# Kernel tuning notes

Measured on AMD Instinct MI355X. Metric: run time of the kernel, lower is better.

The kernel has to match this reference:

```python
import jax, jax.numpy as jnp
import numpy as np

N_ENT = 50000
N_REL = 500
DIM = 256
BATCH = 512
EPS = 1e-5


def setup_inputs() -> dict:
    key = jax.random.key(0)
    ks = jax.random.split(key, 5)
    E_emb = jax.random.normal(ks[0], (4, N_ENT, DIM), jnp.float32)   # (a_re, a_im, b_re, b_im)
    R_emb = jax.random.normal(ks[1], (4, N_REL, DIM), jnp.float32)
    psi_emb = jax.random.normal(ks[2], (N_REL, DIM), jnp.float32)
    bn_gamma = jnp.ones((4, DIM), jnp.float32)
    bn_beta = jnp.zeros((4, DIM), jnp.float32)
    biases = jnp.zeros((4, N_ENT), jnp.float32)                      # b_a, b_x, b_y, b_z
    h_idx = jax.random.randint(ks[3], (BATCH,), 0, N_ENT)
    r_idx = jax.random.randint(ks[4], (BATCH,), 0, N_REL)
    return dict(E_emb=E_emb, R_emb=R_emb, psi_emb=psi_emb, bn_gamma=bn_gamma,
                bn_beta=bn_beta, biases=biases, h_idx=h_idx, r_idx=r_idx)


def _qnorm(q):
    # QubitNorm: normalize so |a|^2 + |b|^2 = 1 per embedding coordinate.
    # q: [4, ..., d] stacked real parts.
    length = jnp.sqrt(jnp.sum(q * q, axis=0, keepdims=True))
    return q / length


def _bn(q, gamma, beta):
    # QubitBatchNorm1d (training-mode batch stats), per component and per feature.
    # q: [4, B, d]
    mean = q.mean(axis=1, keepdims=True)
    var = q.var(axis=1, keepdims=True)
    return (q - mean) / jnp.sqrt(var + EPS) * gamma[:, None, :] + beta[:, None, :]


def _cmul(a, b):
    return (a[0] * b[0] - a[1] * b[1], a[0] * b[1] + a[1] * b[0])


def reference(E_emb, R_emb, psi_emb, bn_gamma, bn_beta, biases, h_idx, r_idx):
    # h = E_bn(norm(E(h_idx)))
    h = _bn(_qnorm(E_emb[:, h_idx]), bn_gamma, bn_beta)   # [4, B, d]
    # r = norm(R(r_idx))
    r = _qnorm(R_emb[:, r_idx])                           # [4, B, d]
    psi = psi_emb[r_idx]                                  # [B, d]
    z = (jnp.cos(psi), jnp.sin(psi))
    h_a, h_b = (h[0], h[1]), (h[2], h[3])
    r_a, r_b = (r[0], r[1]), (r[2], r[3])
    ra_conj = (r[0], -r[1])
    rb_conj = (r[2], -r[3])
    # QubitMult: a = h_a*r_a - z*(h_b*conj(r_b)); b = h_a*r_b + z*(h_b*conj(r_a))
    m1 = _cmul(h_a, r_a)
    m2 = _cmul(z, _cmul(h_b, rb_conj))
    m3 = _cmul(h_a, r_b)
    m4 = _cmul(z, _cmul(h_b, ra_conj))
    t = jnp.stack([m1[0] - m2[0], m1[1] - m2[1], m3[0] + m4[0], m3[1] + m4[1]])  # [4, B, d]
    # All-entity table: E_bn(norm(E))
    E = _bn(_qnorm(E_emb), bn_gamma, bn_beta)             # [4, N, d]
    # QubitScoringAll: per-component dot product against all entities (dropout = eval identity)
    scores = jnp.einsum('cbd,cnd->cbn', t, E)             # [4, B, N]
    y = jax.nn.sigmoid(scores + biases[:, None, :])       # (y_a, y_ai, y_b, y_bi) stacked
    return y
```

## Files before the change

### kernel.cpp

```cpp
#include <hip/hip_runtime.h>
#include <math.h>

#define NENT 50000
#define NREL 500
#define DIM 256
#define BATCH 512
#define EPSV 1e-5f

#define WS_ACC    0
#define WS_STATS  4096
#define WS_KC     8192
#define WS_F16    10240

typedef _Float16 f16x8 __attribute__((ext_vector_type(8)));
typedef _Float16 f16x4 __attribute__((ext_vector_type(4)));
typedef float f32x4 __attribute__((ext_vector_type(4)));
typedef float f32x16 __attribute__((ext_vector_type(16)));

__device__ inline f32x16 zero16() {
    f32x16 v;
#pragma unroll
    for (int i = 0; i < 16; ++i) v[i] = 0.f;
    return v;
}

__global__ void convert_stats_kernel(const float* __restrict__ E, _Float16* __restrict__ Eh,
                                     float* __restrict__ acc) {
    __shared__ float red[3][64][33];
    int tid = threadIdx.x;
    int dq = tid & 63, j = tid >> 6;
    int d0 = dq * 4;
    int per = (NENT + gridDim.x - 1) / gridDim.x;
    int n0 = blockIdx.x * per;
    int n1 = n0 + per; if (n1 > NENT) n1 = NENT;

    float sm[4][4]; float sq[4][4];
#pragma unroll
    for (int c = 0; c < 4; ++c)
#pragma unroll
        for (int dd = 0; dd < 4; ++dd) { sm[c][dd] = 0.f; sq[c][dd] = 0.f; }

    for (int n = n0 + j; n < n1; n += 4) {
        size_t ga = (size_t)n * DIM + d0;
        f32x4 e[4];
        e[0] = *(const f32x4*)(E + ga);
        e[1] = *(const f32x4*)(E + (size_t)NENT * DIM + ga);
        e[2] = *(const f32x4*)(E + (size_t)2 * NENT * DIM + ga);
        e[3] = *(const f32x4*)(E + (size_t)3 * NENT * DIM + ga);
        float inv[4];
#pragma unroll
        for (int dd = 0; dd < 4; ++dd)
            inv[dd] = rsqrtf(e[0][dd]*e[0][dd] + e[1][dd]*e[1][dd] +
                             e[2][dd]*e[2][dd] + e[3][dd]*e[3][dd]);
#pragma unroll
        for (int c = 0; c < 4; ++c) {
            f16x4 hv;
#pragma unroll
            for (int dd = 0; dd < 4; ++dd) {
                float v = e[c][dd] * inv[dd];
                hv[dd] = (_Float16)v;
                sm[c][dd] += v; sq[c][dd] += v * v;
            }
            *(f16x4*)(Eh + (size_t)c * NENT * DIM + ga) = hv;
        }
    }

    if (j > 0) {
        float* p = &red[j-1][dq][0];
#pragma unroll
        for (int c = 0; c < 4; ++c)
#pragma unroll
            for (int dd = 0; dd < 4; ++dd) {
                p[c*4 + dd]      = sm[c][dd];
                p[16 + c*4 + dd] = sq[c][dd];
            }
    }
    __syncthreads();
    if (j == 0) {
#pragma unroll
        for (int c = 0; c < 4; ++c)
#pragma unroll
            for (int dd = 0; dd < 4; ++dd) {
                float s = sm[c][dd] + red[0][dq][c*4+dd] + red[1][dq][c*4+dd] + red[2][dq][c*4+dd];
                float q = sq[c][dd] + red[0][dq][16+c*4+dd] + red[1][dq][16+c*4+dd] + red[2][dq][16+c*4+dd];
                atomicAdd(&acc[c*DIM + d0 + dd], s);
                atomicAdd(&acc[1024 + c*DIM + d0 + dd], q);
            }
    }
}

__global__ void stats_batch_kernel(const float* __restrict__ E, const int* __restrict__ h_idx,
                                   float* __restrict__ accH) {
    int d = threadIdx.x;
    int b0 = blockIdx.x * 32;
    float sm0=0,sm1=0,sm2=0,sm3=0, sq0=0,sq1=0,sq2=0,sq3=0;
    for (int j = 0; j < 32; ++j) {
        int n = h_idx[b0 + j];
        int ga = n*DIM + d;
        float e0 = E[ga];
        float e1 = E[1*NENT*DIM + ga];
        float e2 = E[2*NENT*DIM + ga];
        float e3 = E[3*NENT*DIM + ga];
        float inv = rsqrtf(e0*e0+e1*e1+e2*e2+e3*e3);
        e0*=inv; e1*=inv; e2*=inv; e3*=inv;
        sm0+=e0; sq0+=e0*e0;
        sm1+=e1; sq1+=e1*e1;
        sm2+=e2; sq2+=e2*e2;
        sm3+=e3; sq3+=e3*e3;
    }
    atomicAdd(&accH[0*DIM+d], sm0); atomicAdd(&accH[1024 + 0*DIM+d], sq0);
    atomicAdd(&accH[1*DIM+d], sm1); atomicAdd(&accH[1024 + 1*DIM+d], sq1);
    atomicAdd(&accH[2*DIM+d], sm2); atomicAdd(&accH[1024 + 2*DIM+d], sq2);
    atomicAdd(&accH[3*DIM+d], sm3); atomicAdd(&accH[1024 + 3*DIM+d], sq3);
}

__global__ void finalize_stats_kernel(const float* __restrict__ acc, float* __restrict__ stats) {
    int i = blockIdx.x * blockDim.x + threadIdx.x;
    float mE = acc[i] * (1.0f / NENT);
    float vE = acc[1024 + i] * (1.0f / NENT) - mE * mE;
    float mH = acc[2048 + i] * (1.0f / BATCH);
    float vH = acc[3072 + i] * (1.0f / BATCH) - mH * mH;
    stats[i]        = mE;
    stats[1024 + i] = rsqrtf(vE + EPSV);
    stats[2048 + i] = mH;
    stats[3072 + i] = rsqrtf(vH + EPSV);
}

__global__ void build_t_kernel(const float* __restrict__ E, const float* __restrict__ R,
                               const float* __restrict__ psi_emb,
                               const float* __restrict__ gamma, const float* __restrict__ beta,
                               const int* __restrict__ h_idx, const int* __restrict__ r_idx,
                               const float* __restrict__ stats,
                               _Float16* __restrict__ th, float* __restrict__ Kc) {
    __shared__ float red[4];
    int b = blockIdx.x, d = threadIdx.x;
    int wave = d >> 6, lane = d & 63;
    int hn = h_idx[b], rn = r_idx[b];

    float hv[4];
    hv[0] = E[hn*DIM + d];
    hv[1] = E[1*NENT*DIM + hn*DIM + d];
    hv[2] = E[2*NENT*DIM + hn*DIM + d];
    hv[3] = E[3*NENT*DIM + hn*DIM + d];
    float invh = rsqrtf(hv[0]*hv[0]+hv[1]*hv[1]+hv[2]*hv[2]+hv[3]*hv[3]);
    float hq[4];
#pragma unroll
    for (int c = 0; c < 4; ++c) {
        float v = hv[c] * invh;
        float mH = stats[2048 + c*DIM + d], isH = stats[3072 + c*DIM + d];
        hq[c] = (v - mH) * isH * gamma[c*DIM + d] + beta[c*DIM + d];
    }

    float r0 = R[rn*DIM + d];
    float r1 = R[1*NREL*DIM + rn*DIM + d];
    float r2 = R[2*NREL*DIM + rn*DIM + d];
    float r3 = R[3*NREL*DIM + rn*DIM + d];
    float invr = rsqrtf(r0*r0+r1*r1+r2*r2+r3*r3);
    r0*=invr; r1*=invr; r2*=invr; r3*=invr;

    float p = psi_emb[rn*DIM + d];
    float cz = cosf(p), sz = sinf(p);

    float m1r = hq[0]*r0 - hq[1]*r1;
    float m1i = hq[0]*r1 + hq[1]*r0;
    float X   = hq[2]*r2 + hq[3]*r3;
    float Y   = hq[3]*r2 - hq[2]*r3;
    float m2r = cz*X - sz*Y;
    float m2i = cz*Y + sz*X;
    float m3r = hq[0]*r2 - hq[1]*r3;
    float m3i = hq[0]*r3 + hq[1]*r2;
    float U   = hq[2]*r0 + hq[3]*r1;
    float V   = hq[3]*r0 - hq[2]*r1;
    float m4r = cz*U - sz*V;
    float m4i = cz*V + sz*U;

    float t[4] = { m1r - m2r, m1i - m2i, m3r + m4r, m3i + m4i };

#pragma unroll
    for (int c = 0; c < 4; ++c) {
        float g   = gamma[c*DIM + d];
        float mE  = stats[c*DIM + d];
        float isE = stats[1024 + c*DIM + d];
        th[((size_t)c*BATCH + b)*DIM + d] = (_Float16)(t[c] * g * isE);
        float kp = t[c] * (beta[c*DIM + d] - g * mE * isE);
#pragma unroll
        for (int off = 32; off > 0; off >>= 1) kp += __shfl_down(kp, off, 64);
        if (lane == 0) red[wave] = kp;
        __syncthreads();
        if (d == 0) Kc[c*BATCH + b] = red[0] + red[1] + red[2] + red[3];
        __syncthreads();
    }
}

__launch_bounds__(256)
__global__ void score_gemm_kernel(const _Float16* __restrict__ th,
                                  const _Float16* __restrict__ Eh,
                                  const float* __restrict__ Kc,
                                  const float* __restrict__ biases,
                                  float* __restrict__ out) {
    __shared__ __align__(1024) char smem[32768];
    int tid = threadIdx.x;
    int w = tid >> 6, l = tid & 63;
    int lr = l & 31, lh = l >> 5;
    int wm = w & 1, wn = w >> 1;

    int lin = blockIdx.x + (int)gridDim.x * (blockIdx.y + (int)gridDim.y * blockIdx.z);
    int wg  = (lin & 7) * 782 + (lin >> 3);
    int bt  = wg & 3;
    int nt  = (wg >> 2) % 391;
    int c   = wg / 1564;
    int b0  = bt * 128;
    int n0  = nt * 128;

    const _Float16* Ah = th + (size_t)c * BATCH * DIM;
    const _Float16* Bh = Eh + (size_t)c * NENT * DIM;

    f32x16 acc00 = zero16(), acc01 = zero16(), acc10 = zero16(), acc11 = zero16();

    auto stage = [&](int kc, int slot) {
        int kbase = kc * 32;
#pragma unroll
        for (int i = 0; i < 4; ++i) {
            int f = w * 4 + i;
            const _Float16* gp;
            if (f < 8) {
                int mf = f >> 1, ks = f & 1;
                gp = Ah + (size_t)(b0 + mf*32 + lr) * DIM + kbase + ks*16 + lh*8;
            } else {
                int g = f - 8, nf = g >> 1, ks = g & 1;
                int n = n0 + nf*32 + lr; if (n > NENT-1) n = NENT-1;
                gp = Bh + (size_t)n * DIM + kbase + ks*16 + lh*8;
            }
            __builtin_amdgcn_global_load_lds(
                (const __attribute__((address_space(1))) void*)gp,
                (__attribute__((address_space(3))) void*)(smem + slot * 16384 + f * 1024),
                16, 0, 0);
        }
    };

    auto compute = [&](int slot) {
        const char* s = smem + slot * 16384;
#pragma unroll
        for (int ks = 0; ks < 2; ++ks) {
            f16x8 a0  = *(const f16x8*)(s + ((wm*2+0)*2 + ks)*1024 + l*16);
            f16x8 a1  = *(const f16x8*)(s + ((wm*2+1)*2 + ks)*1024 + l*16);
            f16x8 bb0 = *(const f16x8*)(s + 8192 + ((wn*2+0)*2 + ks)*1024 + l*16);
            f16x8 bb1 = *(const f16x8*)(s + 8192 + ((wn*2+1)*2 + ks)*1024 + l*16);
            acc00 = __builtin_amdgcn_mfma_f32_32x32x16_f16(a0, bb0, acc00, 0, 0, 0);
            acc01 = __builtin_amdgcn_mfma_f32_32x32x16_f16(a0, bb1, acc01, 0, 0, 0);
            acc10 = __builtin_amdgcn_mfma_f32_32x32x16_f16(a1, bb0, acc10, 0, 0, 0);
            acc11 = __builtin_amdgcn_mfma_f32_32x32x16_f16(a1, bb1, acc11, 0, 0, 0);
        }
    };

    stage(0, 0);
    for (int t = 0; t < 7; ++t) {
        stage(t + 1, (t + 1) & 1);
        asm volatile("s_waitcnt vmcnt(4)" ::: "memory");
        __builtin_amdgcn_s_barrier();
        compute(t & 1);
        __builtin_amdgcn_s_barrier();
    }
    asm volatile("s_waitcnt vmcnt(0)" ::: "memory");
    __builtin_amdgcn_s_barrier();
    compute(1);

    const float* Kcc = Kc + c * BATCH;
    const float* bc  = biases + (size_t)c * NENT;
    float* oc = out + (size_t)c * BATCH * NENT;
#pragma unroll
    for (int mi = 0; mi < 2; ++mi) {
#pragma unroll
        for (int ni = 0; ni < 2; ++ni) {
            const f32x16& a = (mi==0) ? (ni==0 ? acc00 : acc01) : (ni==0 ? acc10 : acc11);
            int n = n0 + wn*64 + ni*32 + lr;
            bool ok = (n < NENT);
            float bv = ok ? bc[n] : 0.f;
#pragma unroll
            for (int reg = 0; reg < 16; ++reg) {
                int m = b0 + wm*64 + mi*32 + (reg & 3) + 8*(reg >> 2) + 4*lh;
                float x = a[reg] + Kcc[m] + bv;
                if (ok) oc[(size_t)m * NENT + n] = 1.f / (1.f + __expf(-x));
            }
        }
    }
}

extern "C" void kernel_launch(void* const* d_in, const int* in_sizes, int n_in,
                              void* d_out, int out_size, void* d_ws, size_t ws_size,
                              hipStream_t stream) {
    const float* E      = (const float*)d_in[0];
    const float* R      = (const float*)d_in[1];
    const float* psi    = (const float*)d_in[2];
    const float* gamma  = (const float*)d_in[3];
    const float* beta   = (const float*)d_in[4];
    const float* biases = (const float*)d_in[5];
    const int* h_idx    = (const int*)d_in[6];
    const int* r_idx    = (const int*)d_in[7];
    float* out = (float*)d_out;
    float* ws  = (float*)d_ws;

    _Float16* th = (_Float16*)(ws + WS_F16);
    _Float16* Eh = th + (size_t)4 * BATCH * DIM;

    hipMemsetAsync(ws + WS_ACC, 0, 4096 * sizeof(float), stream);

    convert_stats_kernel<<<512, 256, 0, stream>>>(E, Eh, ws + WS_ACC);
    stats_batch_kernel<<<16, 256, 0, stream>>>(E, h_idx, ws + WS_ACC + 2048);
    finalize_stats_kernel<<<4, 256, 0, stream>>>(ws + WS_ACC, ws + WS_STATS);
    build_t_kernel<<<BATCH, 256, 0, stream>>>(E, R, psi, gamma, beta, h_idx, r_idx,
                                              ws + WS_STATS, th, ws + WS_KC);
    dim3 grid((NENT + 127) / 128, BATCH / 128, 4);
    score_gemm_kernel<<<grid, 256, 0, stream>>>(th, Eh, ws + WS_KC, biases, out);
}
```

Measured before the change: 788.1 us.

## Merge stats kernels, stage Kc in LDS, use nontemporal stores

Folds the batch-statistics kernel into the conversion kernel as extra blocks. The finalize step moves into build_t, so two kernel launches disappear. The GEMM epilogue now preloads the Kc slice into LDS via global_load_lds and prefetches the bias before the main loop. Eh and output writes use nontemporal stores to reduce cache pollution. The goals are less launch overhead and lower epilogue load latency, at the cost of a slightly larger LDS footprint.

```diff
diff --git a/kernel.cpp b/kernel.cpp
--- a/kernel.cpp
+++ b/kernel.cpp
@@ -8,7 +8,6 @@
 #define EPSV 1e-5f
 
 #define WS_ACC    0
-#define WS_STATS  4096
 #define WS_KC     8192
 #define WS_F16    10240
 
@@ -25,12 +24,37 @@
 }
 
 __global__ void convert_stats_kernel(const float* __restrict__ E, _Float16* __restrict__ Eh,
-                                     float* __restrict__ acc) {
+                                     float* __restrict__ acc, const int* __restrict__ h_idx) {
+    if (blockIdx.x >= 512) {
+        int d = threadIdx.x;
+        int b0 = (blockIdx.x - 512) * 32;
+        float sm0=0,sm1=0,sm2=0,sm3=0, sq0=0,sq1=0,sq2=0,sq3=0;
+        for (int j = 0; j < 32; ++j) {
+            int n = h_idx[b0 + j];
+            int ga = n*DIM + d;
+            float e0 = E[ga];
+            float e1 = E[1*NENT*DIM + ga];
+            float e2 = E[2*NENT*DIM + ga];
+            float e3 = E[3*NENT*DIM + ga];
+            float inv = rsqrtf(e0*e0+e1*e1+e2*e2+e3*e3);
+            e0*=inv; e1*=inv; e2*=inv; e3*=inv;
+            sm0+=e0; sq0+=e0*e0;
+            sm1+=e1; sq1+=e1*e1;
+            sm2+=e2; sq2+=e2*e2;
+            sm3+=e3; sq3+=e3*e3;
+        }
+        atomicAdd(&acc[2048 + 0*DIM+d], sm0); atomicAdd(&acc[3072 + 0*DIM+d], sq0);
+        atomicAdd(&acc[2048 + 1*DIM+d], sm1); atomicAdd(&acc[3072 + 1*DIM+d], sq1);
+        atomicAdd(&acc[2048 + 2*DIM+d], sm2); atomicAdd(&acc[3072 + 2*DIM+d], sq2);
+        atomicAdd(&acc[2048 + 3*DIM+d], sm3); atomicAdd(&acc[3072 + 3*DIM+d], sq3);
+        return;
+    }
+
     __shared__ float red[3][64][33];
     int tid = threadIdx.x;
     int dq = tid & 63, j = tid >> 6;
     int d0 = dq * 4;
-    int per = (NENT + gridDim.x - 1) / gridDim.x;
+    int per = (NENT + 511) / 512;
     int n0 = blockIdx.x * per;
     int n1 = n0 + per; if (n1 > NENT) n1 = NENT;
 
@@ -61,7 +85,7 @@
                 hv[dd] = (_Float16)v;
                 sm[c][dd] += v; sq[c][dd] += v * v;
             }
-            *(f16x4*)(Eh + (size_t)c * NENT * DIM + ga) = hv;
+            __builtin_nontemporal_store(hv, (f16x4*)(Eh + (size_t)c * NENT * DIM + ga));
         }
     }
 
@@ -89,53 +113,31 @@
     }
 }
 
-__global__ void stats_batch_kernel(const float* __restrict__ E, const int* __restrict__ h_idx,
-                                   float* __restrict__ accH) {
-    int d = threadIdx.x;
-    int b0 = blockIdx.x * 32;
-    float sm0=0,sm1=0,sm2=0,sm3=0, sq0=0,sq1=0,sq2=0,sq3=0;
-    for (int j = 0; j < 32; ++j) {
-        int n = h_idx[b0 + j];
-        int ga = n*DIM + d;
-        float e0 = E[ga];
-        float e1 = E[1*NENT*DIM + ga];
-        float e2 = E[2*NENT*DIM + ga];
-        float e3 = E[3*NENT*DIM + ga];
-        float inv = rsqrtf(e0*e0+e1*e1+e2*e2+e3*e3);
-        e0*=inv; e1*=inv; e2*=inv; e3*=inv;
-        sm0+=e0; sq0+=e0*e0;
-        sm1+=e1; sq1+=e1*e1;
-        sm2+=e2; sq2+=e2*e2;
-        sm3+=e3; sq3+=e3*e3;
-    }
-    atomicAdd(&accH[0*DIM+d], sm0); atomicAdd(&accH[1024 + 0*DIM+d], sq0);
-    atomicAdd(&accH[1*DIM+d], sm1); atomicAdd(&accH[1024 + 1*DIM+d], sq1);
-    atomicAdd(&accH[2*DIM+d], sm2); atomicAdd(&accH[1024 + 2*DIM+d], sq2);
-    atomicAdd(&accH[3*DIM+d], sm3); atomicAdd(&accH[1024 + 3*DIM+d], sq3);
-}
-
-__global__ void finalize_stats_kernel(const float* __restrict__ acc, float* __restrict__ stats) {
-    int i = blockIdx.x * blockDim.x + threadIdx.x;
-    float mE = acc[i] * (1.0f / NENT);
-    float vE = acc[1024 + i] * (1.0f / NENT) - mE * mE;
-    float mH = acc[2048 + i] * (1.0f / BATCH);
-    float vH = acc[3072 + i] * (1.0f / BATCH) - mH * mH;
-    stats[i]        = mE;
-    stats[1024 + i] = rsqrtf(vE + EPSV);
-    stats[2048 + i] = mH;
-    stats[3072 + i] = rsqrtf(vH + EPSV);
-}
-
 __global__ void build_t_kernel(const float* __restrict__ E, const float* __restrict__ R,
                                const float* __restrict__ psi_emb,
                                const float* __restrict__ gamma, const float* __restrict__ beta,
                                const int* __restrict__ h_idx, const int* __restrict__ r_idx,
-                               const float* __restrict__ stats,
+                               const float* __restrict__ acc,
                                _Float16* __restrict__ th, float* __restrict__ Kc) {
     __shared__ float red[4];
     int b = blockIdx.x, d = threadIdx.x;
     int wave = d >> 6, lane = d & 63;
     int hn = h_idx[b], rn = r_idx[b];
+
+    float mE[4], isE[4], mH[4], isH[4];
+#pragma unroll
+    for (int c = 0; c < 4; ++c) {
+        float a0 = acc[c*DIM + d];
+        float a1 = acc[1024 + c*DIM + d];
+        float a2 = acc[2048 + c*DIM + d];
+        float a3 = acc[3072 + c*DIM + d];
+        mE[c] = a0 * (1.0f / NENT);
+        float vE = a1 * (1.0f / NENT) - mE[c] * mE[c];
+        isE[c] = rsqrtf(vE + EPSV);
+        mH[c] = a2 * (1.0f / BATCH);
+        float vH = a3 * (1.0f / BATCH) - mH[c] * mH[c];
+        isH[c] = rsqrtf(vH + EPSV);
+    }
 
     float hv[4];
     hv[0] = E[hn*DIM + d];
@@ -147,8 +149,7 @@
 #pragma unroll
     for (int c = 0; c < 4; ++c) {
         float v = hv[c] * invh;
-        float mH = stats[2048 + c*DIM + d], isH = stats[3072 + c*DIM + d];
-        hq[c] = (v - mH) * isH * gamma[c*DIM + d] + beta[c*DIM + d];
+        hq[c] = (v - mH[c]) * isH[c] * gamma[c*DIM + d] + beta[c*DIM + d];
     }
 
     float r0 = R[rn*DIM + d];
@@ -179,10 +180,8 @@
 #pragma unroll
     for (int c = 0; c < 4; ++c) {
         float g   = gamma[c*DIM + d];
-        float mE  = stats[c*DIM + d];
-        float isE = stats[1024 + c*DIM + d];
-        th[((size_t)c*BATCH + b)*DIM + d] = (_Float16)(t[c] * g * isE);
-        float kp = t[c] * (beta[c*DIM + d] - g * mE * isE);
+        th[((size_t)c*BATCH + b)*DIM + d] = (_Float16)(t[c] * g * isE[c]);
+        float kp = t[c] * (beta[c*DIM + d] - g * mE[c] * isE[c]);
 #pragma unroll
         for (int off = 32; off > 0; off >>= 1) kp += __shfl_down(kp, off, 64);
         if (lane == 0) red[wave] = kp;
@@ -198,7 +197,7 @@
                                   const float* __restrict__ Kc,
                                   const float* __restrict__ biases,
                                   float* __restrict__ out) {
-    __shared__ __align__(1024) char smem[32768];
+    __shared__ __align__(1024) char smem[32768 + 512];
     int tid = threadIdx.x;
     int w = tid >> 6, l = tid & 63;
     int lr = l & 31, lh = l >> 5;
@@ -214,6 +213,22 @@
 
     const _Float16* Ah = th + (size_t)c * BATCH * DIM;
     const _Float16* Bh = Eh + (size_t)c * NENT * DIM;
+    const float* Kcc = Kc + c * BATCH;
+    const float* bc  = biases + (size_t)c * NENT;
+
+    int ng0 = n0 + wn*64 + lr;
+    int ng1 = ng0 + 32;
+    int ng0c = ng0 > NENT-1 ? NENT-1 : ng0;
+    int ng1c = ng1 > NENT-1 ? NENT-1 : ng1;
+    float bv0 = bc[ng0c];
+    float bv1 = bc[ng1c];
+    if (w < 2) {
+        __builtin_amdgcn_global_load_lds(
+            (const __attribute__((address_space(1))) void*)(Kcc + b0 + w*64 + l),
+            (__attribute__((address_space(3))) void*)(smem + 32768 + w*256),
+            4, 0, 0);
+    }
+    float* kcs = (float*)(smem + 32768);
 
     f32x16 acc00 = zero16(), acc01 = zero16(), acc10 = zero16(), acc11 = zero16();
 
@@ -265,22 +280,21 @@
     __builtin_amdgcn_s_barrier();
     compute(1);
 
-    const float* Kcc = Kc + c * BATCH;
-    const float* bc  = biases + (size_t)c * NENT;
     float* oc = out + (size_t)c * BATCH * NENT;
 #pragma unroll
     for (int mi = 0; mi < 2; ++mi) {
 #pragma unroll
         for (int ni = 0; ni < 2; ++ni) {
             const f32x16& a = (mi==0) ? (ni==0 ? acc00 : acc01) : (ni==0 ? acc10 : acc11);
-            int n = n0 + wn*64 + ni*32 + lr;
+            int n = ni == 0 ? ng0 : ng1;
             bool ok = (n < NENT);
-            float bv = ok ? bc[n] : 0.f;
+            float bv = ni == 0 ? bv0 : bv1;
 #pragma unroll
             for (int reg = 0; reg < 16; ++reg) {
-                int m = b0 + wm*64 + mi*32 + (reg & 3) + 8*(reg >> 2) + 4*lh;
-                float x = a[reg] + Kcc[m] + bv;
-                if (ok) oc[(size_t)m * NENT + n] = 1.f / (1.f + __expf(-x));
+                int mloc = wm*64 + mi*32 + (reg & 3) + 8*(reg >> 2) + 4*lh;
+                float x = a[reg] + kcs[mloc] + bv;
+                float y = 1.f / (1.f + __expf(-x));
+                if (ok) __builtin_nontemporal_store(y, &oc[(size_t)(b0 + mloc) * NENT + n]);
             }
         }
     }
@@ -305,11 +319,9 @@
 
     hipMemsetAsync(ws + WS_ACC, 0, 4096 * sizeof(float), stream);
 
-    convert_stats_kernel<<<512, 256, 0, stream>>>(E, Eh, ws + WS_ACC);
-    stats_batch_kernel<<<16, 256, 0, stream>>>(E, h_idx, ws + WS_ACC + 2048);
-    finalize_stats_kernel<<<4, 256, 0, stream>>>(ws + WS_ACC, ws + WS_STATS);
+    convert_stats_kernel<<<528, 256, 0, stream>>>(E, Eh, ws + WS_ACC, h_idx);
     build_t_kernel<<<BATCH, 256, 0, stream>>>(E, R, psi, gamma, beta, h_idx, r_idx,
-                                              ws + WS_STATS, th, ws + WS_KC);
+                                              ws + WS_ACC, th, ws + WS_KC);
     dim3 grid((NENT + 127) / 128, BATCH / 128, 4);
     score_gemm_kernel<<<grid, 256, 0, stream>>>(th, Eh, ws + WS_KC, biases, out);
 }
```

After: 769.5 us. 1.02x faster.
